# Optimization experiments

Hardware: AMD Instinct MI355X
Metric: run time of the kernel (lower is better)

The kernel has to match this reference:

```python
import jax, jax.numpy as jnp
import numpy as np

B, L, C, H, K, P = 64, 2048, 128, 128, 64, 336
NUM_BLOCKS = 4
EPS = 1e-5


def _revin_norm(x):
    mean = jnp.mean(x, axis=1, keepdims=True)
    std = jnp.sqrt(jnp.var(x, axis=1, keepdims=True) + EPS)
    return (x - mean) / std, mean, std


def _bn(x, gamma, beta, ch_axis):
    # training-mode BatchNorm1d: stats over all axes except ch_axis
    axes = tuple(i for i in range(x.ndim) if i != ch_axis)
    mean = jnp.mean(x, axis=axes, keepdims=True)
    var = jnp.var(x, axis=axes, keepdims=True)
    shp = [1] * x.ndim
    shp[ch_axis] = -1
    return (x - mean) / jnp.sqrt(var + EPS) * gamma.reshape(shp) + beta.reshape(shp)


def _mixer_block(x, bn_t_g, bn_t_b, lin_t_w, lin_t_b, bn_f_g, bn_f_b,
                 lin_f1_w, lin_f1_b, lin_f2_w, lin_f2_b):
    # timestep mixer: BN treats seq dim as channels, Linear over seq dim
    y = _bn(x, bn_t_g, bn_t_b, 1)                       # [B,L,C]
    y = jnp.swapaxes(y, 1, 2)                           # [B,C,L]
    y = jax.nn.gelu(y @ lin_t_w + lin_t_b, approximate=False)
    y = jnp.swapaxes(y, 1, 2)
    x = x + y
    # feature mixer: BN over channel dim, 2-layer MLP over features
    y = jnp.swapaxes(x, 1, 2)                           # [B,C,L]
    y = _bn(y, bn_f_g, bn_f_b, 1)
    y = jnp.swapaxes(y, 1, 2)                           # [B,L,C]
    y = jax.nn.gelu(y @ lin_f1_w + lin_f1_b, approximate=False)
    y = y @ lin_f2_w + lin_f2_b
    return x + y


def _forward(x, bern_u, cluster_embeds, wq_w, wq_b, wk_w, wk_b, wv_w, wv_b,
             cm_w1, cm_b1, cm_w2, cm_b2, tm_w1, tm_b1, tm_w2, tm_b2,
             bn_t_g, bn_t_b, lin_t_w, lin_t_b, bn_f_g, bn_f_b,
             lin_f1_w, lin_f1_b, lin_f2_w, lin_f2_b, out_w, out_b):
    xn, _, _ = _revin_norm(x)                           # [B,L,C]
    # channel MLP -> token embeddings h_i
    h = jax.nn.relu(xn @ cm_w1 + cm_b1) @ cm_w2 + cm_b2  # [B,L,H]
    # cosine-similarity soft routing to codebook
    hn = h / (jnp.linalg.norm(h, axis=-1, keepdims=True) + 1e-8)
    cn = cluster_embeds / (jnp.linalg.norm(cluster_embeds, axis=-1, keepdims=True) + 1e-8)
    p = jax.nn.softmax(jnp.einsum('blh,kh->blk', hn, cn), axis=-1)   # [B,L,K]
    M = (bern_u < p).astype(x.dtype)                    # bernoulli sample via external uniforms
    # exp-attention between cluster queries and token keys, masked by M
    Q = cluster_embeds @ wq_w + wq_b                    # [K,H]
    Km = h @ wk_w + wk_b                                # [B,L,H]
    V = h @ wv_w + wv_b                                 # [B,L,H]
    scores = jnp.einsum('kh,blh->bkl', Q, Km) / jnp.sqrt(jnp.asarray(H, x.dtype))
    aw = jax.nn.softmax(jnp.exp(scores) * jnp.swapaxes(M, 1, 2), axis=-1)  # [B,K,L]
    ao = jnp.einsum('bkl,blh->bkh', aw, V)              # [B,K,H]
    upd = ao * jnp.mean(p, axis=1)[:, :, None]          # prob-weighted cluster update
    new_cluster_embeds = jnp.mean(upd, axis=0)          # [K,H] (EMA-style copy target)
    # temporal module on channel embeddings
    h2 = jax.nn.relu(h @ tm_w1 + tm_b1) @ tm_w2 + tm_b2  # [B,L,H], H==C
    z, mean2, std2 = _revin_norm(h2)                    # second 'norm' overwrites stats
    for _ in range(NUM_BLOCKS):
        z = _mixer_block(z, bn_t_g, bn_t_b, lin_t_w, lin_t_b,
                         bn_f_g, bn_f_b, lin_f1_w, lin_f1_b, lin_f2_w, lin_f2_b)
    y = jnp.swapaxes(jnp.swapaxes(z, 1, 2) @ out_w + out_b, 1, 2)    # [B,P,C]
    y = y * std2 + mean2                                # denorm with second-call stats
    return y, new_cluster_embeds


def setup_inputs() -> dict:
    key = jax.random.key(0)
    ks = iter(jax.random.split(key, 40))

    def lin_w(fan_in, shape):
        return jax.random.uniform(next(ks), shape, jnp.float32, -1.0, 1.0) / np.sqrt(fan_in).astype(np.float32)

    return {
        'x': jax.random.normal(next(ks), (B, L, C), jnp.float32),
        'bern_u': jax.random.uniform(next(ks), (B, L, K), jnp.float32),
        'cluster_embeds': jax.random.normal(next(ks), (K, H), jnp.float32),
        'wq_w': lin_w(H, (H, H)), 'wq_b': lin_w(H, (H,)),
        'wk_w': lin_w(H, (H, H)), 'wk_b': lin_w(H, (H,)),
        'wv_w': lin_w(H, (H, H)), 'wv_b': lin_w(H, (H,)),
        'cm_w1': lin_w(C, (C, H)), 'cm_b1': lin_w(C, (H,)),
        'cm_w2': lin_w(H, (H, H)), 'cm_b2': lin_w(H, (H,)),
        'tm_w1': lin_w(H, (H, H)), 'tm_b1': lin_w(H, (H,)),
        'tm_w2': lin_w(H, (H, H)), 'tm_b2': lin_w(H, (H,)),
        'bn_t_g': jnp.ones((L,), jnp.float32), 'bn_t_b': jnp.zeros((L,), jnp.float32),
        'lin_t_w': lin_w(L, (L, L)), 'lin_t_b': lin_w(L, (L,)),
        'bn_f_g': jnp.ones((C,), jnp.float32), 'bn_f_b': jnp.zeros((C,), jnp.float32),
        'lin_f1_w': lin_w(C, (C, H)), 'lin_f1_b': lin_w(C, (H,)),
        'lin_f2_w': lin_w(H, (H, C)), 'lin_f2_b': lin_w(H, (C,)),
        'out_w': lin_w(L, (L, P)), 'out_b': lin_w(L, (P,)),
    }


def reference(x, bern_u, cluster_embeds, wq_w, wq_b, wk_w, wk_b, wv_w, wv_b,
              cm_w1, cm_b1, cm_w2, cm_b2, tm_w1, tm_b1, tm_w2, tm_b2,
              bn_t_g, bn_t_b, lin_t_w, lin_t_b, bn_f_g, bn_f_b,
              lin_f1_w, lin_f1_b, lin_f2_w, lin_f2_b, out_w, out_b):
    return _forward(x, bern_u, cluster_embeds, wq_w, wq_b, wk_w, wk_b, wv_w, wv_b,
                    cm_w1, cm_b1, cm_w2, cm_b2, tm_w1, tm_b1, tm_w2, tm_b2,
                    bn_t_g, bn_t_b, lin_t_w, lin_t_b, bn_f_g, bn_f_b,
                    lin_f1_w, lin_f1_b, lin_f2_w, lin_f2_b, out_w, out_b)
```

## Files before the change

### kernel.cpp

```cpp
#include <hip/hip_runtime.h>
#include <math.h>

#define BB 64
#define LL 2048
#define CC 128
#define HH 128
#define KK 64
#define PP 336
#define EPSf 1e-5f

typedef __attribute__((ext_vector_type(8))) short short8v;
typedef __attribute__((ext_vector_type(4))) float float4v;

__device__ inline ushort f2bf(float f) {
    union { float f; unsigned u; } v; v.f = f;
    unsigned r = (v.u + 0x7FFFu + ((v.u >> 16) & 1u)) >> 16;
    return (ushort)r;
}
__device__ inline float bf2f(ushort h) {
    union { unsigned u; float f; } v; v.u = ((unsigned)h) << 16;
    return v.f;
}

__device__ inline float fast_gelu(float v) {
// ... 119 lines not shown
            *(float4*)&Ws[kr][nc] = v;
        }
        __syncthreads();
        #pragma unroll
        for (int k = 0; k < 32; ++k) {
            float a[8], w[8];
            *(float4*)&a[0] = *(const float4*)&As[k][ty * 8];
            *(float4*)&a[4] = *(const float4*)&As[k][ty * 8 + 4];
            *(float4*)&w[0] = *(const float4*)&Ws[k][tx * 4];
            *(float4*)&w[4] = *(const float4*)&Ws[k][64 + tx * 4];
            #pragma unroll
            for (int i = 0; i < 8; ++i)
                #pragma unroll
                for (int j = 0; j < 8; ++j)
                    acc[i][j] = fmaf(a[i], w[j], acc[i][j]);
        }
    }

    #pragma unroll
    for (int i = 0; i < 8; ++i) {
        int m = m0 + ty * 8 + i;
        if (m >= M) continue;
        #pragma unroll
        for (int jj = 0; jj < 8; jj += 4) {
            int n = n0 + (jj ? 64 + tx * 4 : tx * 4);
            if (n >= N) continue;
            float o[4];
            #pragma unroll
            for (int j = 0; j < 4; ++j)
                o[j] = acc[i][jj + j] + (bias ? bias[n + j] : 0.f);
            *(float4*)(Out + (size_t)m * ldo + n) = *(float4*)o;
        }
    }
}

template <int NORM, int ACT, int EP>
__global__ __launch_bounds__(512)
void mfma_sq_kernel(const float* __restrict__ A, const ushort* __restrict__ Whi,
                    const ushort* __restrict__ Wlo, const float* __restrict__ bias,
                    float* Out,
                    const float* __restrict__ nmu, const float* __restrict__ ns,
                    const float* __restrict__ nt, int normStride,
                    ushort* __restrict__ hbOut) {
    __shared__ ushort Ahi[128][72];
    __shared__ ushort Alo[128][72];
    __shared__ ushort Bhi[128][72];
    __shared__ ushort Blo[128][72];
    int tid = threadIdx.x;
    int m0 = blockIdx.x * 128;
    int noff = (NORM == 1) ? (m0 / LL) * normStride : 0;

    int w = tid >> 6, lane = tid & 63;
    int wm = (w >> 1) * 32, wn = (w & 1) * 64;
    int col = lane & 15, kq = lane >> 4;

    float4v acc[2][4];
    #pragma unroll
    for (int i = 0; i < 2; ++i)
        #pragma unroll
        for (int j = 0; j < 4; ++j) acc[i][j] = (float4v){0.f, 0.f, 0.f, 0.f};

    for (int kt = 0; kt < 2; ++kt) {
        __syncthreads();
        #pragma unroll
        for (int it = 0; it < 2; ++it) {
            int q = tid + it * 512;
            int row = q >> 3, k0 = (q & 7) * 8;
            int kg = kt * 64 + k0;
            const float* ap = A + (size_t)(m0 + row) * 128 + kg;
            float vv[8];
            *(float4*)&vv[0] = *(const float4*)ap;
            *(float4*)&vv[4] = *(const float4*)(ap + 4);
            ushort hi[8], lo[8];
            #pragma unroll
            for (int j = 0; j < 8; ++j) {
                float v = vv[j];
                if (NORM == 1) v = (v - nmu[noff + kg + j]) * ns[noff + kg + j];
                if (NORM == 2) v = (v - nmu[kg + j]) * ns[kg + j] + nt[kg + j];
                ushort h = f2bf(v);
                hi[j] = h;
                lo[j] = f2bf(v - bf2f(h));
            }
            if (hbOut)
                *(short8v*)(hbOut + (size_t)(m0 + row) * 128 + kg) = *(short8v*)hi;
            *(short8v*)&Ahi[row][k0] = *(short8v*)hi;
            *(short8v*)&Alo[row][k0] = *(short8v*)lo;
        }
        #pragma unroll
        for (int it = 0; it < 2; ++it) {
            int q = tid + it * 512;
            int row = q >> 3, k0 = (q & 7) * 8;
            *(short8v*)&Bhi[row][k0] =
                *(const short8v*)(Whi + (size_t)row * 128 + kt * 64 + k0);
            *(short8v*)&Blo[row][k0] =
                *(const short8v*)(Wlo + (size_t)row * 128 + kt * 64 + k0);
        }
        __syncthreads();
        #pragma unroll
        for (int ksub = 0; ksub < 2; ++ksub) {
            short8v ah[2], al[2], bh[4], bl[4];
            #pragma unroll
            for (int mf = 0; mf < 2; ++mf) {
                ah[mf] = *(const short8v*)&Ahi[wm + mf * 16 + col][ksub * 32 + kq * 8];
                al[mf] = *(const short8v*)&Alo[wm + mf * 16 + col][ksub * 32 + kq * 8];
            }
            #pragma unroll
            for (int nf = 0; nf < 4; ++nf) {
                bh[nf] = *(const short8v*)&Bhi[wn + nf * 16 + col][ksub * 32 + kq * 8];
                bl[nf] = *(const short8v*)&Blo[wn + nf * 16 + col][ksub * 32 + kq * 8];
            }
            #pragma unroll
            for (int mf = 0; mf < 2; ++mf)
                #pragma unroll
                for (int nf = 0; nf < 4; ++nf)
                    acc[mf][nf] = __builtin_amdgcn_mfma_f32_16x16x32_bf16(
                        ah[mf], bh[nf], acc[mf][nf], 0, 0, 0);
            #pragma unroll
            for (int mf = 0; mf < 2; ++mf)
                #pragma unroll
                for (int nf = 0; nf < 4; ++nf)
                    acc[mf][nf] = __builtin_amdgcn_mfma_f32_16x16x32_bf16(
                        ah[mf], bl[nf], acc[mf][nf], 0, 0, 0);
            #pragma unroll
            for (int mf = 0; mf < 2; ++mf)
                #pragma unroll
                for (int nf = 0; nf < 4; ++nf)
                    acc[mf][nf] = __builtin_amdgcn_mfma_f32_16x16x32_bf16(
                        al[mf], bh[nf], acc[mf][nf], 0, 0, 0);
        }
    }

    int rbase = kq * 4;
    #pragma unroll
    for (int nf = 0; nf < 4; ++nf) {
        int n = wn + nf * 16 + col;
        if (EP == 2 && n >= 64) continue;
        float bn = bias ? bias[n] : 0.f;
        #pragma unroll
        for (int mf = 0; mf < 2; ++mf) {
            #pragma unroll
            for (int r = 0; r < 4; ++r) {
                int m = m0 + wm + mf * 16 + rbase + r;
                float v = acc[mf][nf][r] + bn;
                if (ACT == 1) v = fmaxf(v, 0.f);
                if (ACT == 2) v = fast_gelu(v);
                if (EP == 0) Out[(size_t)m * 128 + n] = v;
                else if (EP == 1) Out[(size_t)m * 128 + n] += v;
                else Out[(size_t)m * 64 + n] = v;
            }
        }
    }
}

template <int NORM, int ACT1, int ACT2, int EP2, int PREC>
__global__ __launch_bounds__(512)
void mfma_sq2_kernel(const float* __restrict__ A,
                     const ushort* __restrict__ W1h, const ushort* __restrict__ W1l,
                     const float* __restrict__ b1v,
                     const ushort* __restrict__ W2h, const ushort* __restrict__ W2l,
                     const float* __restrict__ b2v, float* Out,
                     const float* __restrict__ nmu, const float* __restrict__ ns,
                     const float* __restrict__ nt, int normStride,
                     float* __restrict__ rsum, float* __restrict__ rsq) {
    __shared__ ushort Xhi[128][72];
    __shared__ ushort Xlo[PREC ? 128 : 1][72];
    __shared__ ushort Bh[128][72];
    __shared__ ushort Bl[PREC ? 128 : 1][72];
    int tid = threadIdx.x;
    int m0 = blockIdx.x * 128;
    int noff = (NORM == 1) ? (m0 / LL) * normStride : 0;
    int w = tid >> 6, lane = tid & 63;
    int wm = (w >> 1) * 32, wn = (w & 1) * 64;
    int col = lane & 15, kq = lane >> 4;

    float4v acc[2][4];
    #pragma unroll
    for (int i = 0; i < 2; ++i)
        #pragma unroll
        for (int j = 0; j < 4; ++j) acc[i][j] = (float4v){0.f, 0.f, 0.f, 0.f};

    for (int kt = 0; kt < 2; ++kt) {
        __syncthreads();
        #pragma unroll
        for (int it = 0; it < 2; ++it) {
            int q = tid + it * 512;
            int row = q >> 3, k0 = (q & 7) * 8;
            int kg = kt * 64 + k0;
            const float* ap = A + (size_t)(m0 + row) * 128 + kg;
            float vv[8];
            *(float4*)&vv[0] = *(const float4*)ap;
            *(float4*)&vv[4] = *(const float4*)(ap + 4);
            ushort hi[8], lo[8];
            #pragma unroll
            for (int j = 0; j < 8; ++j) {
                float v = vv[j];
                if (NORM == 1) v = (v - nmu[noff + kg + j]) * ns[noff + kg + j];
                if (NORM == 2) v = (v - nmu[kg + j]) * ns[kg + j] + nt[kg + j];
                ushort h = f2bf(v);
                hi[j] = h;
                if (PREC) lo[j] = f2bf(v - bf2f(h));
            }
            *(short8v*)&Xhi[row][k0] = *(short8v*)hi;
            if (PREC) *(short8v*)&Xlo[row][k0] = *(short8v*)lo;
        }
        #pragma unroll
        for (int it = 0; it < 2; ++it) {
            int q = tid + it * 512;
            int row = q >> 3, k0 = (q & 7) * 8;
            *(short8v*)&Bh[row][k0] =
                *(const short8v*)(W1h + (size_t)row * 128 + kt * 64 + k0);
            if (PREC)
                *(short8v*)&Bl[row][k0] =
                    *(const short8v*)(W1l + (size_t)row * 128 + kt * 64 + k0);
        }
        __syncthreads();
        #pragma unroll
        for (int ksub = 0; ksub < 2; ++ksub) {
            short8v ah[2], al[2], bh[4], bl[4];
            #pragma unroll
            for (int mf = 0; mf < 2; ++mf) {
                ah[mf] = *(const short8v*)&Xhi[wm + mf * 16 + col][ksub * 32 + kq * 8];
                if (PREC) al[mf] = *(const short8v*)&Xlo[wm + mf * 16 + col][ksub * 32 + kq * 8];
            }
            #pragma unroll
            for (int nf = 0; nf < 4; ++nf) {
                bh[nf] = *(const short8v*)&Bh[wn + nf * 16 + col][ksub * 32 + kq * 8];
                if (PREC) bl[nf] = *(const short8v*)&Bl[wn + nf * 16 + col][ksub * 32 + kq * 8];
            }
            #pragma unroll
            for (int mf = 0; mf < 2; ++mf)
                #pragma unroll
                for (int nf = 0; nf < 4; ++nf)
                    acc[mf][nf] = __builtin_amdgcn_mfma_f32_16x16x32_bf16(
                        ah[mf], bh[nf], acc[mf][nf], 0, 0, 0);
            if (PREC) {
                #pragma unroll
                for (int mf = 0; mf < 2; ++mf)
                    #pragma unroll
                    for (int nf = 0; nf < 4; ++nf)
                        acc[mf][nf] = __builtin_amdgcn_mfma_f32_16x16x32_bf16(
                            ah[mf], bl[nf], acc[mf][nf], 0, 0, 0);
                #pragma unroll
                for (int mf = 0; mf < 2; ++mf)
                    #pragma unroll
                    for (int nf = 0; nf < 4; ++nf)
                        acc[mf][nf] = __builtin_amdgcn_mfma_f32_16x16x32_bf16(
                            al[mf], bh[nf], acc[mf][nf], 0, 0, 0);
            }
        }
    }

    float4v acc2[2][4];
    #pragma unroll
    for (int i = 0; i < 2; ++i)
        #pragma unroll
        for (int j = 0; j < 4; ++j) acc2[i][j] = (float4v){0.f, 0.f, 0.f, 0.f};

    for (int kt2 = 0; kt2 < 2; ++kt2) {
        __syncthreads();
        if ((wn >> 6) == kt2) {
            #pragma unroll
            for (int nf = 0; nf < 4; ++nf) {
                float bn = b1v[wn + nf * 16 + col];
                #pragma unroll
                for (int mf = 0; mf < 2; ++mf) {
                    #pragma unroll
                    for (int r = 0; r < 4; ++r) {
                        float v = acc[mf][nf][r] + bn;
                        if (ACT1 == 1) v = fmaxf(v, 0.f);
                        if (ACT1 == 2) v = fast_gelu(v);
                        int row = wm + mf * 16 + kq * 4 + r;
                        int c2 = nf * 16 + col;
                        ushort h = f2bf(v);
                        Xhi[row][c2] = h;
                        if (PREC) Xlo[row][c2] = f2bf(v - bf2f(h));
                    }
                }
            }
        }
        #pragma unroll
        for (int it = 0; it < 2; ++it) {
            int q = tid + it * 512;
            int row = q >> 3, k0 = (q & 7) * 8;
            *(short8v*)&Bh[row][k0] =
                *(const short8v*)(W2h + (size_t)row * 128 + kt2 * 64 + k0);
            if (PREC)
                *(short8v*)&Bl[row][k0] =
                    *(const short8v*)(W2l + (size_t)row * 128 + kt2 * 64 + k0);
        }
        __syncthreads();
        #pragma unroll
        for (int ksub = 0; ksub < 2; ++ksub) {
            short8v ah[2], al[2], bh[4], bl[4];
            #pragma unroll
            for (int mf = 0; mf < 2; ++mf) {
                ah[mf] = *(const short8v*)&Xhi[wm + mf * 16 + col][ksub * 32 + kq * 8];
                if (PREC) al[mf] = *(const short8v*)&Xlo[wm + mf * 16 + col][ksub * 32 + kq * 8];
            }
            #pragma unroll
            for (int nf = 0; nf < 4; ++nf) {
                bh[nf] = *(const short8v*)&Bh[wn + nf * 16 + col][ksub * 32 + kq * 8];
                if (PREC) bl[nf] = *(const short8v*)&Bl[wn + nf * 16 + col][ksub * 32 + kq * 8];
            }
            #pragma unroll
            for (int mf = 0; mf < 2; ++mf)
                #pragma unroll
                for (int nf = 0; nf < 4; ++nf)
                    acc2[mf][nf] = __builtin_amdgcn_mfma_f32_16x16x32_bf16(
                        ah[mf], bh[nf], acc2[mf][nf], 0, 0, 0);
            if (PREC) {
                #pragma unroll
                for (int mf = 0; mf < 2; ++mf)
                    #pragma unroll
                    for (int nf = 0; nf < 4; ++nf)
                        acc2[mf][nf] = __builtin_amdgcn_mfma_f32_16x16x32_bf16(
                            ah[mf], bl[nf], acc2[mf][nf], 0, 0, 0);
                #pragma unroll
                for (int mf = 0; mf < 2; ++mf)
                    #pragma unroll
                    for (int nf = 0; nf < 4; ++nf)
                        acc2[mf][nf] = __builtin_amdgcn_mfma_f32_16x16x32_bf16(
                            al[mf], bh[nf], acc2[mf][nf], 0, 0, 0);
            }
        }
    }

    int rbase = kq * 4;
    float rs_[2][4];
    float rq_[2][4];
    float cs_[4], cq_[4];
    if (EP2 == 1 || EP2 == 3) {
        #pragma unroll
        for (int a = 0; a < 2; ++a)
            #pragma unroll
            for (int b = 0; b < 4; ++b) { rs_[a][b] = 0.f; rq_[a][b] = 0.f; }
    }
    if (EP2 == 2) {
        #pragma unroll
        for (int a = 0; a < 4; ++a) { cs_[a] = 0.f; cq_[a] = 0.f; }
    }
    #pragma unroll
    for (int nf = 0; nf < 4; ++nf) {
        int n = wn + nf * 16 + col;
        float bn = b2v[n];
        #pragma unroll
        for (int mf = 0; mf < 2; ++mf) {
            #pragma unroll
            for (int r = 0; r < 4; ++r) {
                int m = m0 + wm + mf * 16 + rbase + r;
                float v = acc2[mf][nf][r] + bn;
                if (ACT2 == 1) v = fmaxf(v, 0.f);
                if (ACT2 == 2) v = fast_gelu(v);
                if (EP2 == 1) {
                    float fin = Out[(size_t)m * 128 + n] + v;
                    Out[(size_t)m * 128 + n] = fin;
                    rs_[mf][r] += fin;
                    rq_[mf][r] += fin * fin;
                } else {
                    Out[(size_t)m * 128 + n] = v;
                    if (EP2 == 2) { cs_[nf] += v; cq_[nf] += v * v; }
                    if (EP2 == 3) rq_[mf][r] += v * v;
                }
            }
        }
    }
    if (EP2 == 1) {
        #pragma unroll
        for (int mf = 0; mf < 2; ++mf)
            #pragma unroll
            for (int r = 0; r < 4; ++r) {
                float s = rs_[mf][r], q = rq_[mf][r];
                #pragma unroll
                for (int o = 1; o <= 8; o <<= 1) {
                    s += __shfl_xor(s, o);
                    q += __shfl_xor(q, o);
                }
                rs_[mf][r] = s; rq_[mf][r] = q;
            }
        __syncthreads();
        float* sred = (float*)&Xhi[0][0];
        float* qred = sred + 256;
        if (col == 0) {
            #pragma unroll
            for (int mf = 0; mf < 2; ++mf)
                #pragma unroll
                for (int r = 0; r < 4; ++r) {
                    int row = wm + mf * 16 + kq * 4 + r;
                    sred[row * 2 + (wn >> 6)] = rs_[mf][r];
                    qred[row * 2 + (wn >> 6)] = rq_[mf][r];
                }
        }
        __syncthreads();
        if (tid < 128) {
            rsum[(size_t)m0 + tid] = sred[tid * 2] + sred[tid * 2 + 1];
            rsq[(size_t)m0 + tid]  = qred[tid * 2] + qred[tid * 2 + 1];
        }
    }
    if (EP2 == 3) {
        #pragma unroll
        for (int mf = 0; mf < 2; ++mf)
            #pragma unroll
            for (int r = 0; r < 4; ++r) {
                float q = rq_[mf][r];
                #pragma unroll
                for (int o = 1; o <= 8; o <<= 1) q += __shfl_xor(q, o);
                rq_[mf][r] = q;
            }
        __syncthreads();
        float* qred = (float*)&Xhi[0][0];
        if (col == 0) {
            #pragma unroll
            for (int mf = 0; mf < 2; ++mf)
                #pragma unroll
                for (int r = 0; r < 4; ++r) {
                    int row = wm + mf * 16 + kq * 4 + r;
                    qred[row * 2 + (wn >> 6)] = rq_[mf][r];
                }
        }
        __syncthreads();
        if (tid < 128)
            rsq[(size_t)m0 + tid] = qred[tid * 2] + qred[tid * 2 + 1];
    }
    if (EP2 == 2) {
        #pragma unroll
        for (int nf = 0; nf < 4; ++nf) {
            #pragma unroll
            for (int o = 16; o <= 32; o <<= 1) {
                cs_[nf] += __shfl_xor(cs_[nf], o);
                cq_[nf] += __shfl_xor(cq_[nf], o);
            }
        }
        __syncthreads();
        float* colS = (float*)&Xhi[0][0];
        float* colQ = colS + 512;
        if (kq == 0) {
            #pragma unroll
            for (int nf = 0; nf < 4; ++nf) {
                int n = wn + nf * 16 + col;
                colS[(wm >> 5) * 128 + n] = cs_[nf];
                colQ[(wm >> 5) * 128 + n] = cq_[nf];
            }
        }
        __syncthreads();
        if (tid < 128) {
            rsum[(size_t)blockIdx.x * 256 + tid] =
                (colS[tid] + colS[128 + tid]) + (colS[256 + tid] + colS[384 + tid]);
            rsum[(size_t)blockIdx.x * 256 + 128 + tid] =
                (colQ[tid] + colQ[128 + tid]) + (colQ[256 + tid] + colQ[384 + tid]);
        }
    }
}

__global__ void wsplit_kernel(const float* __restrict__ W, ushort* __restrict__ Whi,
                              ushort* __restrict__ Wlo) {
    __shared__ float t[32][33];
    int k0 = blockIdx.x * 32, n0 = blockIdx.y * 32;
    int tx = threadIdx.x, ty = threadIdx.y;
    for (int i = ty; i < 32; i += 8)
        t[i][tx] = W[(size_t)(k0 + i) * 128 + n0 + tx];
    __syncthreads();
    for (int i = ty; i < 32; i += 8) {
        float v = t[tx][i];
        ushort h = f2bf(v);
        Whi[(size_t)(n0 + i) * 128 + k0 + tx] = h;
        Wlo[(size_t)(n0 + i) * 128 + k0 + tx] = f2bf(v - bf2f(h));
    }
}

__global__ __launch_bounds__(512)
void mfma_ts5_kernel(const ushort* __restrict__ A, const ushort* __restrict__ W,
                     const float* __restrict__ bias, float* Z,
                     int nx, int nwg, float* __restrict__ bnfP) {
    __shared__ __align__(16) ushort smem[32768];
    float (*Ol)[132] = (float(*)[132])smem;

    int bid = blockIdx.x;
    int cpx = nwg >> 3;
    int swz = (bid & 7) * cpx + (bid >> 3);
    int n0 = (swz % nx) * 128;
    int m0 = (swz / nx) * 128;

    int tid = threadIdx.x;
    int w = tid >> 6, lane = tid & 63;
    int wm = (w >> 1) * 32, wn = (w & 1) * 64;
    int col = lane & 15, kq = lane >> 4;

    int srow = lane >> 3;
    int scol = ((lane & 7) ^ srow) << 3;
    int xr = (col & 7) << 4;

    float4v acc[2][4];
    #pragma unroll
    for (int i = 0; i < 2; ++i)
        #pragma unroll
        for (int j = 0; j < 4; ++j) acc[i][j] = (float4v){0.f, 0.f, 0.f, 0.f};

    const int Kd = LL;
    const int kTiles = 32;

    #pragma unroll
    for (int it = 0; it < 2; ++it) {
        int rb = (w << 4) + (it << 3);
        async16(A + (size_t)(m0 + rb + srow) * Kd + scol, smem + (rb << 6));
        async16(W + (size_t)(n0 + rb + srow) * Kd + scol, smem + 8192 + (rb << 6));
    }
    __syncthreads();

    for (int kt = 0; kt < kTiles; ++kt) {
        int cur = kt & 1;
        const ushort* Ac = smem + (cur << 14);
        const ushort* Bc = Ac + 8192;
        if (kt + 1 < kTiles) {
            ushort* An = smem + ((cur ^ 1) << 14);
            ushort* Bn = An + 8192;
            int kb = (kt + 1) << 6;
            #pragma unroll
            for (int it = 0; it < 2; ++it) {
                int rb = (w << 4) + (it << 3);
                async16(A + (size_t)(m0 + rb + srow) * Kd + kb + scol, An + (rb << 6));
                async16(W + (size_t)(n0 + rb + srow) * Kd + kb + scol, Bn + (rb << 6));
            }
        }
        __builtin_amdgcn_s_setprio(1);
        #pragma unroll
        for (int ksub = 0; ksub < 2; ++ksub) {
            int cswz = (((ksub << 6) + (kq << 4)) ^ xr) >> 1;
            short8v af[2], bf[4];
            #pragma unroll
            for (int mf = 0; mf < 2; ++mf)
                af[mf] = *(const short8v*)(Ac + (wm + mf * 16 + col) * 64 + cswz);
            #pragma unroll
            for (int nf = 0; nf < 4; ++nf)
                bf[nf] = *(const short8v*)(Bc + (wn + nf * 16 + col) * 64 + cswz);
            #pragma unroll
            for (int mf = 0; mf < 2; ++mf)
                #pragma unroll
                for (int nf = 0; nf < 4; ++nf)
                    acc[mf][nf] = __builtin_amdgcn_mfma_f32_16x16x32_bf16(
                        af[mf], bf[nf], acc[mf][nf], 0, 0, 0);
        }
        __builtin_amdgcn_s_setprio(0);
        __syncthreads();
    }

    int b = m0 >> 7;
    float cs[8], cq[8];
    #pragma unroll
    for (int j = 0; j < 8; ++j) { cs[j] = 0.f; cq[j] = 0.f; }
// ... 33 lines not shown
        }
    }
    __syncthreads();
    float* sred = (float*)smem;
    float* qred = sred + 4096;
    #pragma unroll
    for (int j = 0; j < 8; ++j) {
        sred[nloc * 128 + c0 + j] = cs[j];
        qred[nloc * 128 + c0 + j] = cq[j];
    }
    __syncthreads();
    if (tid < 128) {
        float a = 0.f;
        for (int r = 0; r < 32; ++r) a += sred[r * 128 + tid];
        bnfP[(size_t)bid * 256 + tid] = a;
    } else if (tid < 256) {
        int c = tid - 128;
        float a = 0.f;
        for (int r = 0; r < 32; ++r) a += qred[r * 128 + c];
        bnfP[(size_t)bid * 256 + 128 + c] = a;
    }
}

template <int EPM>
__global__ __launch_bounds__(512)
void mfma_g8_kernel(const ushort* __restrict__ A, const ushort* __restrict__ W,
                    const float* __restrict__ bias, float* Z,
                    int N, int Kd, int LDO, int nx, int nwg,
                    const float* __restrict__ epS, const float* __restrict__ epM) {
    __shared__ __align__(16) ushort smem[32768];
    float (*Ol)[132] = (float(*)[132])smem;

    int bid = blockIdx.x;
    int cpx = nwg >> 3;
    int swz = (bid & 7) * cpx + (bid >> 3);
    int n0 = (swz % nx) * 128;
    int m0 = (swz / nx) * 128;

    int tid = threadIdx.x;
    int w = tid >> 6, lane = tid & 63;
    int wm = (w >> 1) * 32, wn = (w & 1) * 64;
    int col = lane & 15, kq = lane >> 4;

    int srow = lane >> 3;
    int scol = ((lane & 7) ^ srow) << 3;
    int xr = (col & 7) << 4;

    float4v acc[2][4];
    #pragma unroll
    for (int i = 0; i < 2; ++i)
        #pragma unroll
        for (int j = 0; j < 4; ++j) acc[i][j] = (float4v){0.f, 0.f, 0.f, 0.f};

    int kTiles = Kd >> 6;

    #pragma unroll
    for (int it = 0; it < 2; ++it) {
        int rb = (w << 4) + (it << 3);
        async16(A + (size_t)(m0 + rb + srow) * Kd + scol, smem + (rb << 6));
        async16(W + (size_t)(n0 + rb + srow) * Kd + scol, smem + 8192 + (rb << 6));
    }
    __syncthreads();

    for (int kt = 0; kt < kTiles; ++kt) {
        int cur = kt & 1;
        const ushort* Ac = smem + (cur << 14);
        const ushort* Bc = Ac + 8192;
        if (kt + 1 < kTiles) {
            ushort* An = smem + ((cur ^ 1) << 14);
            ushort* Bn = An + 8192;
            int kb = (kt + 1) << 6;
            #pragma unroll
            for (int it = 0; it < 2; ++it) {
                int rb = (w << 4) + (it << 3);
                async16(A + (size_t)(m0 + rb + srow) * Kd + kb + scol, An + (rb << 6));
                async16(W + (size_t)(n0 + rb + srow) * Kd + kb + scol, Bn + (rb << 6));
            }
        }
        __builtin_amdgcn_s_setprio(1);
        #pragma unroll
        for (int ksub = 0; ksub < 2; ++ksub) {
            int cswz = (((ksub << 6) + (kq << 4)) ^ xr) >> 1;
            short8v af[2], bf[4];
            #pragma unroll
            for (int mf = 0; mf < 2; ++mf)
                af[mf] = *(const short8v*)(Ac + (wm + mf * 16 + col) * 64 + cswz);
            #pragma unroll
            for (int nf = 0; nf < 4; ++nf)
                bf[nf] = *(const short8v*)(Bc + (wn + nf * 16 + col) * 64 + cswz);
            #pragma unroll
            for (int mf = 0; mf < 2; ++mf)
                #pragma unroll
                for (int nf = 0; nf < 4; ++nf)
                    acc[mf][nf] = __builtin_amdgcn_mfma_f32_16x16x32_bf16(
                        af[mf], bf[nf], acc[mf][nf], 0, 0, 0);
        }
        __builtin_amdgcn_s_setprio(0);
        __syncthreads();
    }

    int b = m0 >> 7;
    int nloc = tid >> 4, c0 = (tid & 15) * 8;
    #pragma unroll
    for (int q = 0; q < 4; ++q) {
        __syncthreads();
        #pragma unroll
        for (int nf = 0; nf < 4; ++nf) {
            int gnl = wn + nf * 16;
            if ((gnl >> 5) != q) continue;
            int gn = n0 + gnl + col;
            float bn = (EPM == 2 && gn >= N) ? 0.f : bias[gn];
            int nl = gnl - q * 32 + col;
            #pragma unroll
            for (int mf = 0; mf < 2; ++mf)
                #pragma unroll
                for (int r = 0; r < 4; ++r)
                    Ol[nl][wm + mf * 16 + kq * 4 + r] = acc[mf][nf][r] + bn;
        }
        __syncthreads();
        int gn = n0 + q * 32 + nloc;
        if (gn >= N) continue;
        float* zr;
        if (EPM == 3)
            zr = Z + (((size_t)(m0 >> 11) * 64 + gn) * 2048) + (m0 & 2047) + c0;
        else
            zr = Z + ((size_t)b * LDO + gn) * CC + c0;
        #pragma unroll
        for (int i = 0; i < 2; ++i) {
            float4 v = *(float4*)&Ol[nloc][c0 + i * 4];
            if (EPM == 2) {
                int mb = m0 + c0 + i * 4;
                float4 s4 = *(const float4*)(epS + mb);
                float4 m4 = *(const float4*)(epM + mb);
                v.x = v.x * s4.x + m4.x; v.y = v.y * s4.y + m4.y;
                v.z = v.z * s4.z + m4.z; v.w = v.w * s4.w + m4.w;
            }
            *(float4*)(zr + i * 4) = v;
        }
    }
}

__global__ void wtrans_kernel(const float* __restrict__ W, ushort* __restrict__ WT,
                              int Kd, int N) {
    __shared__ float t[32][33];
    int k0 = blockIdx.x * 32, n0 = blockIdx.y * 32;
    int tx = threadIdx.x, ty = threadIdx.y;
    for (int i = ty; i < 32; i += 8) {
        int n = n0 + tx;
        t[i][tx] = (n < N) ? W[(size_t)(k0 + i) * N + n] : 0.f;
    }
    __syncthreads();
    for (int i = ty; i < 32; i += 8)
        WT[(size_t)(n0 + i) * Kd + k0 + tx] = f2bf(t[tx][i]);
}

__global__ void cn_split_kernel(const float* __restrict__ ce, ushort* __restrict__ ch,
                                ushort* __restrict__ cl) {
    int k = blockIdx.x, h = threadIdx.x;
    if (k >= KK) {
        ch[(size_t)k * 128 + h] = 0;
        cl[(size_t)k * 128 + h] = 0;
        return;
    }
    __shared__ float sh[128];
    float v = ce[(size_t)k * HH + h];
    sh[h] = v * v;
    __syncthreads();
    for (int o = 64; o >= 1; o >>= 1) {
        if (h < o) sh[h] += sh[h + o];
        __syncthreads();
    }
    float nv = v / (sqrtf(sh[0]) + 1e-8f);
    ushort hh = f2bf(nv);
    ch[(size_t)k * 128 + h] = hh;
    cl[(size_t)k * 128 + h] = f2bf(nv - bf2f(hh));
}

__global__ void qprime_kernel(const float* __restrict__ Q, const float* __restrict__ wk_w,
                              const float* __restrict__ wk_b, ushort* __restrict__ qpb,
                              float* __restrict__ qbp) {
    int k = blockIdx.x;
    int hp = threadIdx.x;
    if (k >= KK) {
        qpb[(size_t)k * HH + hp] = 0;
        if (hp == 0) qbp[k] = 0.f;
        return;
    }
    __shared__ float qrow[128];
    __shared__ float red[128];
    qrow[hp] = Q[(size_t)k * HH + hp];
    __syncthreads();
    float s = 0.f;
    for (int h = 0; h < HH; ++h) s = fmaf(qrow[h], wk_w[(size_t)hp * HH + h], s);
    const float rs = 0.088388347648318447f;
    qpb[(size_t)k * HH + hp] = f2bf(s * rs);
    red[hp] = qrow[hp] * wk_b[hp];
    __syncthreads();
    for (int o = 64; o >= 1; o >>= 1) {
        if (hp < o) red[hp] += red[hp + o];
        __syncthreads();
    }
    if (hp == 0) qbp[k] = red[0] * rs;
}

__global__ __launch_bounds__(256)
void pmask_kernel(const float* __restrict__ sp, const float* __restrict__ rn,
                  const float* __restrict__ bern, unsigned char* __restrict__ Mt,
                  float* __restrict__ ppart) {
    int b = blockIdx.y;
    int l0 = blockIdx.x * 32;
    int tid = threadIdx.x;
    int wv = tid >> 6, lane = tid & 63;
    __shared__ float Msh[64][33];
    __shared__ float psum[4][64];
    float pa = 0.f;
    for (int tt = 0; tt < 8; ++tt) {
        int l = l0 + wv * 8 + tt;
        size_t tok = (size_t)b * LL + l;
        float s = sp[tok * 64 + lane] * rn[tok];
        float mx = s;
        #pragma unroll
        for (int o = 32; o >= 1; o >>= 1) mx = fmaxf(mx, __shfl_xor(mx, o));
        float ev = expf(s - mx);
        float sm = ev;
        #pragma unroll
        for (int o = 32; o >= 1; o >>= 1) sm += __shfl_xor(sm, o);
        float p = ev / sm;
        pa += p;
        Msh[lane][wv * 8 + tt] = (bern[tok * KK + lane] < p) ? 1.f : 0.f;
    }
    psum[wv][lane] = pa;
    __syncthreads();
    for (int q = tid; q < 64 * 32; q += 256) {
        int k = q >> 5, j = q & 31;
        Mt[((size_t)b * KK + k) * LL + l0 + j] = (unsigned char)Msh[k][j];
    }
    if (tid < 64)
        ppart[((size_t)b * (LL / 32) + blockIdx.x) * KK + tid] =
            psum[0][tid] + psum[1][tid] + psum[2][tid] + psum[3][tid];
}

__global__ void pmean_final_kernel(const float* __restrict__ part, float* __restrict__ pm) {
    int b = blockIdx.x, k = threadIdx.x;
    float s = 0.f;
    for (int i = 0; i < LL / 32; ++i) s += part[((size_t)b * (LL / 32) + i) * KK + k];
    pm[b * KK + k] = s * (1.f / LL);
}

__global__ __launch_bounds__(256)
void aw_kernel(float* __restrict__ S, const unsigned char* __restrict__ Mt) {
    size_t base = (size_t)blockIdx.x * LL;
    int tid = threadIdx.x;
    float t[8];
    float mx = -1e30f;
    #pragma unroll
    for (int i = 0; i < 8; ++i) {
        int l = tid + i * 256;
        float v = expf(S[base + l]) * (float)Mt[base + l];
        t[i] = v;
        mx = fmaxf(mx, v);
    }
    __shared__ float shA[4];
    __shared__ float shB[4];
    #pragma unroll
    for (int o = 32; o >= 1; o >>= 1) mx = fmaxf(mx, __shfl_xor(mx, o));
    if ((tid & 63) == 0) shA[tid >> 6] = mx;
    __syncthreads();
    mx = fmaxf(fmaxf(shA[0], shA[1]), fmaxf(shA[2], shA[3]));
    float e[8];
    float sum = 0.f;
    #pragma unroll
    for (int i = 0; i < 8; ++i) { e[i] = expf(t[i] - mx); sum += e[i]; }
    #pragma unroll
    for (int o = 32; o >= 1; o >>= 1) sum += __shfl_xor(sum, o);
    if ((tid & 63) == 0) shB[tid >> 6] = sum;
    __syncthreads();
    sum = (shB[0] + shB[1]) + (shB[2] + shB[3]);
    float inv = 1.f / sum;
    #pragma unroll
    for (int i = 0; i < 8; ++i) S[base + tid + i * 256] = e[i] * inv;
}

__global__ __launch_bounds__(256)
void awh_part_kernel(const float* __restrict__ AWs, const float* __restrict__ hmat,
                     float* __restrict__ part) {
    __shared__ float AT[32][64];
    __shared__ float VT[32][128];
    int b = blockIdx.y, sp = blockIdx.x;
    int tid = threadIdx.x;
    int tx = tid & 15, ty = tid >> 4;
    float acc[4][8] = {};
    const float* Ab = AWs + (size_t)b * KK * LL + sp * 512;
    const float* Vb = hmat + ((size_t)b * LL + sp * 512) * HH;
    for (int lt = 0; lt < 512; lt += 32) {
        __syncthreads();
        #pragma unroll
        for (int it = 0; it < 2; ++it) {
            int q = tid + it * 256;
            int row = q >> 3;
            int lq = (q & 7) << 2;
            float4 v = *(const float4*)(Ab + (size_t)row * LL + lt + lq);
            AT[lq][row] = v.x; AT[lq + 1][row] = v.y;
            AT[lq + 2][row] = v.z; AT[lq + 3][row] = v.w;
        }
        #pragma unroll
        for (int it = 0; it < 4; ++it) {
            int q = tid + it * 256;
            int lr = q >> 5;
            int hc = (q & 31) << 2;
            *(float4*)&VT[lr][hc] = *(const float4*)(Vb + (size_t)(lt + lr) * HH + hc);
        }
        __syncthreads();
        #pragma unroll
        for (int l = 0; l < 32; ++l) {
            float av[4], vv[8];
            *(float4*)&av[0] = *(const float4*)&AT[l][ty * 4];
            *(float4*)&vv[0] = *(const float4*)&VT[l][tx * 4];
            *(float4*)&vv[4] = *(const float4*)&VT[l][64 + tx * 4];
            #pragma unroll
            for (int i = 0; i < 4; ++i)
                #pragma unroll
                for (int j = 0; j < 8; ++j)
                    acc[i][j] = fmaf(av[i], vv[j], acc[i][j]);
        }
    }
    #pragma unroll
    for (int i = 0; i < 4; ++i) {
        int k = ty * 4 + i;
        #pragma unroll
        for (int jj = 0; jj < 8; jj += 4) {
            int h = (jj ? 64 + tx * 4 : tx * 4);
            float o[4];
            #pragma unroll
            for (int j = 0; j < 4; ++j) o[j] = acc[i][jj + j];
            *(float4*)(part + (((size_t)b * 4 + sp) * KK + k) * HH + h) = *(float4*)o;
        }
    }
}

__global__ void awh_reduce_kernel(const float* __restrict__ part, float* __restrict__ awh) {
    int bk = blockIdx.x, h = threadIdx.x;
    int b = bk >> 6, k = bk & 63;
    float s = 0.f;
    #pragma unroll
    for (int sp = 0; sp < 4; ++sp)
        s += part[(((size_t)b * 4 + sp) * KK + k) * HH + h];
    awh[(size_t)bk * HH + h] = s;
}

__global__ void newce_kernel(const float* __restrict__ ao, const float* __restrict__ pm,
                             float* __restrict__ outTail) {
    int k = blockIdx.x, h = threadIdx.x;
    float s = 0.f;
    for (int b = 0; b < BB; ++b)
        s += ao[((size_t)b * KK + k) * HH + h] * pm[b * KK + k];
    outTail[(size_t)k * HH + h] = s * (1.f / BB);
}

__global__ void revin_apply_kernel(const float* __restrict__ in, float* __restrict__ out,
                                   const float* __restrict__ mu, const float* __restrict__ rs,
                                   float* __restrict__ rsum, float* __restrict__ rsq) {
    int b = blockIdx.y;
    size_t base = (size_t)b * LL * CC + (size_t)blockIdx.x * 8192;
    int c0 = (threadIdx.x * 4) & 127;
    int lane = threadIdx.x & 63;
    float4 m4 = *(const float4*)(mu + b * CC + c0);
    float4 r4 = *(const float4*)(rs + b * CC + c0);
    #pragma unroll
    for (int j = 0; j < 8; ++j) {
        float4 v = *(const float4*)(in + base + threadIdx.x * 4 + j * 1024);
        v.x = (v.x - m4.x) * r4.x; v.y = (v.y - m4.y) * r4.y;
        v.z = (v.z - m4.z) * r4.z; v.w = (v.w - m4.w) * r4.w;
        *(float4*)(out + base + threadIdx.x * 4 + j * 1024) = v;
        float s = v.x + v.y + v.z + v.w;
        float q = v.x * v.x + v.y * v.y + v.z * v.z + v.w * v.w;
        #pragma unroll
        for (int o = 1; o <= 16; o <<= 1) {
            s += __shfl_xor(s, o);
            q += __shfl_xor(q, o);
        }
        if ((lane & 31) == 0) {
            size_t row = (base + (size_t)threadIdx.x * 4 + (size_t)j * 1024) >> 7;
            rsum[row] = s;
            rsq[row] = q;
        }
    }
}

__global__ void bnt_final_kernel(const float* __restrict__ rsum, const float* __restrict__ rsq,
                                 float* __restrict__ mu, float* __restrict__ rv) {
    int l = blockIdx.x * 256 + threadIdx.x;
    float s = 0.f, q = 0.f;
    for (int b = 0; b < BB; ++b) {
        s += rsum[(size_t)b * LL + l];
        q += rsq[(size_t)b * LL + l];
    }
    float m = s * (1.f / (BB * CC));
    float var = q * (1.f / (BB * CC)) - m * m;
    var = fmaxf(var, 0.f);
    mu[l] = m;
    rv[l] = 1.f / sqrtf(var + EPSf);
}

template <bool DO_BN>
__global__ __launch_bounds__(256)
void transpose_bn_kernel(const float* __restrict__ in, ushort* __restrict__ out,
                         const float* __restrict__ mu, const float* __restrict__ rv,
                         const float* __restrict__ g, const float* __restrict__ be) {
    __shared__ ushort tile[32][72];
    int l0 = blockIdx.x * 64, c0 = blockIdx.y * 32, b = blockIdx.z;
    int t = threadIdx.x;
    const float* ib = in + ((size_t)b * LL + l0) * CC + c0;
    #pragma unroll
    for (int it = 0; it < 2; ++it) {
        int idx = t + it * 256;
        int row = idx >> 3;
        int c = (idx & 7) * 4;
        float4 v = *(const float4*)(ib + (size_t)row * CC + c);
        if (DO_BN) {
            int l = l0 + row;
            float sc = rv[l] * g[l];
            float m = mu[l], bb = be[l];
            v.x = (v.x - m) * sc + bb; v.y = (v.y - m) * sc + bb;
            v.z = (v.z - m) * sc + bb; v.w = (v.w - m) * sc + bb;
        }
        tile[c    ][row] = f2bf(v.x);
        tile[c + 1][row] = f2bf(v.y);
        tile[c + 2][row] = f2bf(v.z);
        tile[c + 3][row] = f2bf(v.w);
    }
    __syncthreads();
    int cc = t >> 3, l8 = (t & 7) * 8;
    ushort* ob = out + (size_t)b * CC * LL + (size_t)(c0 + cc) * LL + l0 + l8;
    *(uint4*)ob = *(const uint4*)&tile[cc][l8];
}

__global__ void bnf_mid_kernel(const float* __restrict__ part, float* __restrict__ mid) {
    int gblk = blockIdx.x, t = threadIdx.x;
    float s = 0.f;
    #pragma unroll
    for (int i = 0; i < 16; ++i)
        s += part[(size_t)(gblk * 16 + i) * 256 + t];
    mid[(size_t)gblk * 256 + t] = s;
}

__global__ void bnf_final_kernel(const float* __restrict__ mid, const float* __restrict__ g,
                                 const float* __restrict__ be, float* __restrict__ mu,
                                 float* __restrict__ sA, float* __restrict__ tA) {
    int c = threadIdx.x;
    float s = 0.f, s2 = 0.f;
    #pragma unroll
    for (int i = 0; i < 64; ++i) {
        s += mid[(size_t)i * 256 + c];
        s2 += mid[(size_t)i * 256 + 128 + c];
    }
    float m = s / (float)(BB * LL);
    float var = s2 / (float)(BB * LL) - m * m;
    var = fmaxf(var, 0.f);
    float rvv = 1.f / sqrtf(var + EPSf);
    mu[c] = m;
    sA[c] = rvv * g[c];
    tA[c] = be[c];
}

extern "C" void kernel_launch(void* const* d_in, const int* in_sizes, int n_in,
                              void* d_out, int out_size, void* d_ws, size_t ws_size,
                              hipStream_t stream) {
    const float* x     = (const float*)d_in[0];
    const float* bern  = (const float*)d_in[1];
    const float* ce    = (const float*)d_in[2];
    const float* wq_w  = (const float*)d_in[3];
    const float* wq_b  = (const float*)d_in[4];
    const float* wk_w  = (const float*)d_in[5];
    const float* wk_b  = (const float*)d_in[6];
    const float* wv_w  = (const float*)d_in[7];
    const float* wv_b  = (const float*)d_in[8];
    const float* cm_w1 = (const float*)d_in[9];
    const float* cm_b1 = (const float*)d_in[10];
    const float* cm_w2 = (const float*)d_in[11];
    const float* cm_b2 = (const float*)d_in[12];
    const float* tm_w1 = (const float*)d_in[13];
    const float* tm_b1 = (const float*)d_in[14];
    const float* tm_w2 = (const float*)d_in[15];
    const float* tm_b2 = (const float*)d_in[16];
    const float* bn_t_g = (const float*)d_in[17];
    const float* bn_t_b = (const float*)d_in[18];
    const float* lin_t_w = (const float*)d_in[19];
    const float* lin_t_b = (const float*)d_in[20];
    const float* bn_f_g = (const float*)d_in[21];
    const float* bn_f_b = (const float*)d_in[22];
    const float* f1_w  = (const float*)d_in[23];
    const float* f1_b  = (const float*)d_in[24];
    const float* f2_w  = (const float*)d_in[25];
    const float* f2_b  = (const float*)d_in[26];
    const float* out_w = (const float*)d_in[27];
    const float* out_b = (const float*)d_in[28];
    (void)in_sizes; (void)n_in; (void)out_size;

    float* y = (float*)d_out;
    float* ceOut = y + (size_t)BB * PP * CC;

    float* ws = (float*)d_ws;
    size_t off = 0;
    auto alloc = [&](size_t n) { float* p = ws + off; off += n; return p; };
    float* mean1  = alloc(BB * CC);
    float* rstd1  = alloc(BB * CC);
    float* std1   = alloc(BB * CC);
    float* mean2  = alloc(BB * CC);
    float* rstd2  = alloc(BB * CC);
    float* std2   = alloc(BB * CC);
    float* bnmu   = alloc(LL);
    float* bnrv   = alloc(LL);
    float* bfpart = alloc(1024 * 256);
    float* bfmid  = alloc(64 * 256);
    float* bfmu   = alloc(CC);
    float* bfs    = alloc(CC);
    float* bft    = alloc(CC);
    float* cxpart = alloc(BB * 8 * 256);
    float* cpart2 = alloc(1024 * 256);
    float* qbuf   = alloc(KK * HH);
    ushort* qpb   = (ushort*)alloc(128 * 128 / 2);
    float* qbp    = alloc(128);
    ushort* cnbh  = (ushort*)alloc(8192);
    ushort* cnbl  = (ushort*)alloc(8192);
    float* rn     = alloc((size_t)BB * LL);
    float* rsum   = alloc((size_t)BB * LL);
    float* rsq    = alloc((size_t)BB * LL);
    float* ppart  = alloc((size_t)BB * (LL / 32) * KK);
    float* pmean  = alloc(BB * KK);
    float* awhprt = alloc((size_t)BB * 4 * KK * HH);
    float* awh    = alloc((size_t)BB * KK * HH);
    float* aobuf  = alloc((size_t)BB * KK * HH);
    ushort* wsp   = (ushort*)alloc(7 * 2 * 16384 / 2);
    ushort* wtT   = (ushort*)alloc((size_t)LL * LL / 2);
    ushort* owT   = (ushort*)alloc((size_t)384 * LL / 2);
    float* S      = alloc((size_t)BB * KK * LL);
    float* buf0   = alloc((size_t)BB * LL * CC);
    float* buf2   = alloc((size_t)BB * LL * CC);
    unsigned char* Mt = (unsigned char*)(ws + off);
    ushort* abf = (ushort*)S;
    ushort* hb  = (ushort*)buf0;
    (void)ws_size;

    auto whi = [&](int i) { return wsp + (size_t)i * 2 * 16384; };
    auto wlo = [&](int i) { return wsp + (size_t)i * 2 * 16384 + 16384; };

    const int ML = BB * LL;
    dim3 tb(32, 8);
    dim3 tgrid(LL / 64, CC / 32, BB);
    dim3 wsg(4, 4);

    wtrans_kernel<<<dim3(LL / 32, LL / 32), tb, 0, stream>>>(lin_t_w, wtT, LL, LL);
    wtrans_kernel<<<dim3(LL / 32, 12), tb, 0, stream>>>(out_w, owT, LL, PP);
    wsplit_kernel<<<wsg, tb, 0, stream>>>(cm_w1, whi(0), wlo(0));
    wsplit_kernel<<<wsg, tb, 0, stream>>>(cm_w2, whi(1), wlo(1));
    wsplit_kernel<<<wsg, tb, 0, stream>>>(tm_w1, whi(2), wlo(2));
    wsplit_kernel<<<wsg, tb, 0, stream>>>(tm_w2, whi(3), wlo(3));
    wsplit_kernel<<<wsg, tb, 0, stream>>>(f1_w, whi(4), wlo(4));
    wsplit_kernel<<<wsg, tb, 0, stream>>>(f2_w, whi(5), wlo(5));
    wsplit_kernel<<<wsg, tb, 0, stream>>>(wv_w, whi(6), wlo(6));

    colstats_part_kernel<<<dim3(8, BB), 256, 0, stream>>>(x, cxpart);
    colstats_final_kernel<<<dim3(BB), dim3(128), 0, stream>>>(cxpart, mean1, rstd1, std1);
    mfma_sq2_kernel<1, 1, 0, 3, 1><<<dim3(ML / 128), 512, 0, stream>>>(
        x, whi(0), wlo(0), cm_b1, whi(1), wlo(1), cm_b2, buf2, mean1, rstd1, nullptr, CC,
        nullptr, rsq);
    rn_final_kernel<<<dim3(ML / 256), 256, 0, stream>>>(rsq, rn);
    gemm_kernel<<<dim3(1, 1), 256, 0, stream>>>(ce, wq_w, wq_b, qbuf,
        KK, HH, HH, HH, HH, HH);
    qprime_kernel<<<dim3(128), dim3(128), 0, stream>>>(qbuf, wk_w, wk_b, qpb, qbp);
    cn_split_kernel<<<dim3(128), dim3(128), 0, stream>>>(ce, cnbh, cnbl);
    mfma_sq_kernel<0, 0, 2><<<dim3(ML / 128), 512, 0, stream>>>(
        buf2, cnbh, cnbl, nullptr, S, nullptr, nullptr, nullptr, 0, hb);
    pmask_kernel<<<dim3(LL / 32, BB), 256, 0, stream>>>(S, rn, bern, Mt, ppart);
    pmean_final_kernel<<<dim3(BB), dim3(64), 0, stream>>>(ppart, pmean);
    mfma_g8_kernel<3><<<dim3(1024), 512, 0, stream>>>(
        hb, qpb, qbp, S, KK, 128, 0, 1, 1024, nullptr, nullptr);
    aw_kernel<<<dim3(BB * KK), 256, 0, stream>>>(S, Mt);
    awh_part_kernel<<<dim3(4, BB), 256, 0, stream>>>(S, buf2, awhprt);
    awh_reduce_kernel<<<dim3(BB * KK), dim3(128), 0, stream>>>(awhprt, awh);
    mfma_sq_kernel<0, 0, 0><<<dim3((BB * KK) / 128), 512, 0, stream>>>(
        awh, whi(6), wlo(6), wv_b, aobuf, nullptr, nullptr, nullptr, 0, nullptr);
    newce_kernel<<<dim3(KK), dim3(128), 0, stream>>>(aobuf, pmean, ceOut);
    mfma_sq2_kernel<0, 1, 0, 2, 1><<<dim3(ML / 128), 512, 0, stream>>>(
        buf2, whi(2), wlo(2), tm_b1, whi(3), wlo(3), tm_b2, buf0,
        nullptr, nullptr, nullptr, 0, cpart2, nullptr);
    colstats2_final_kernel<<<dim3(BB), dim3(128), 0, stream>>>(cpart2, mean2, rstd2, std2);
    revin_apply_kernel<<<dim3(32, BB), 256, 0, stream>>>(buf0, buf2, mean2, rstd2, rsum, rsq);
    for (int blkI = 0; blkI < 4; ++blkI) {
        bnt_final_kernel<<<dim3(8), 256, 0, stream>>>(rsum, rsq, bnmu, bnrv);
        transpose_bn_kernel<true><<<tgrid, 256, 0, stream>>>(buf2, abf, bnmu, bnrv, bn_t_g, bn_t_b);
        mfma_ts5_kernel<<<dim3(1024), 512, 0, stream>>>(
            abf, wtT, lin_t_b, buf2, 16, 1024, bfpart);
        bnf_mid_kernel<<<dim3(64), 256, 0, stream>>>(bfpart, bfmid);
        bnf_final_kernel<<<dim3(1), dim3(128), 0, stream>>>(bfmid, bn_f_g, bn_f_b, bfmu, bfs, bft);
        mfma_sq2_kernel<2, 2, 0, 1, 0><<<dim3(ML / 128), 512, 0, stream>>>(
            buf2, whi(4), wlo(4), f1_b, whi(5), wlo(5), f2_b, buf2, bfmu, bfs, bft, 0,
            rsum, rsq);
    }
    transpose_bn_kernel<false><<<tgrid, 256, 0, stream>>>(buf2, abf,
        nullptr, nullptr, nullptr, nullptr);
    mfma_g8_kernel<2><<<dim3(192), 512, 0, stream>>>(
        abf, owT, out_b, y, PP, LL, PP, 3, 192, std2, mean2);
}
```

Measured before the change: 1.161 ms.

## Fold timestep BatchNorm into weights and emit transposed bf16 from feature-mixer epilogue

The per-block timestep BatchNorm scale is folded into a per-iteration scaled copy of the transposed lin_t weight, and its shift into a precomputed bias (W·shift + b). The raw activation therefore no longer needs normalizing. The feature-mixer MLP epilogue now writes the transposed bf16 activation directly through a shared-memory tile. This removes the separate transpose_bn pass over the full B·L·C tensor in each block. In exchange, each block rescales the 2048x2048 bf16 weight (reading and writing about 8MB) and does an extra bias reduction, and the scale is rounded into bf16 weights, which slightly changes numerics.

```diff
diff --git a/kernel.cpp b/kernel.cpp
--- a/kernel.cpp
+++ b/kernel.cpp
@@ -295,7 +295,7 @@
     }
 }
 
-template <int NORM, int ACT1, int ACT2, int EP2, int PREC>
+template <int NORM, int ACT1, int ACT2, int EP2, int PREC, int EMITT>
 __global__ __launch_bounds__(512)
 void mfma_sq2_kernel(const float* __restrict__ A,
                      const ushort* __restrict__ W1h, const ushort* __restrict__ W1l,
@@ -304,11 +304,13 @@
                      const float* __restrict__ b2v, float* Out,
                      const float* __restrict__ nmu, const float* __restrict__ ns,
                      const float* __restrict__ nt, int normStride,
-                     float* __restrict__ rsum, float* __restrict__ rsq) {
+                     float* __restrict__ rsum, float* __restrict__ rsq,
+                     ushort* __restrict__ abfT) {
     __shared__ ushort Xhi[128][72];
     __shared__ ushort Xlo[PREC ? 128 : 1][72];
     __shared__ ushort Bh[128][72];
     __shared__ ushort Bl[PREC ? 128 : 1][72];
+    __shared__ ushort Tbuf[EMITT ? 128 : 1][136];
     int tid = threadIdx.x;
     int m0 = blockIdx.x * 128;
     int noff = (NORM == 1) ? (m0 / LL) * normStride : 0;
@@ -497,6 +499,7 @@
                 if (EP2 == 1) {
                     float fin = Out[(size_t)m * 128 + n] + v;
                     Out[(size_t)m * 128 + n] = fin;
+                    if (EMITT) Tbuf[n][wm + mf * 16 + rbase + r] = f2bf(fin);
                     rs_[mf][r] += fin;
                     rq_[mf][r] += fin * fin;
                 } else {
@@ -537,6 +540,16 @@
         if (tid < 128) {
             rsum[(size_t)m0 + tid] = sred[tid * 2] + sred[tid * 2 + 1];
             rsq[(size_t)m0 + tid]  = qred[tid * 2] + qred[tid * 2 + 1];
+        }
+        if (EMITT) {
+            int bT = m0 >> 11, l0 = m0 & 2047;
+            #pragma unroll
+            for (int it = 0; it < 4; ++it) {
+                int idx = tid + it * 512;
+                int cr = idx >> 4, u = (idx & 15) * 8;
+                *(uint4*)(abfT + ((size_t)bT * CC + cr) * LL + l0 + u) =
+                    *(const uint4*)&Tbuf[cr][u];
+            }
         }
     }
     if (EP2 == 3) {
@@ -876,6 +889,41 @@
     __syncthreads();
     for (int i = ty; i < 32; i += 8)
         WT[(size_t)(n0 + i) * Kd + k0 + tx] = f2bf(t[tx][i]);
+}
+
+__global__ void wtfold_kernel(const ushort* __restrict__ wtT, const float* __restrict__ sc,
+                              ushort* __restrict__ wtTs) {
+    int n = blockIdx.x;
+    int l = threadIdx.x * 8;
+    ushort u[8];
+    *(uint4*)u = *(const uint4*)(wtT + (size_t)n * LL + l);
+    float4 s0 = *(const float4*)(sc + l);
+    float4 s1 = *(const float4*)(sc + l + 4);
+    u[0] = f2bf(bf2f(u[0]) * s0.x); u[1] = f2bf(bf2f(u[1]) * s0.y);
+    u[2] = f2bf(bf2f(u[2]) * s0.z); u[3] = f2bf(bf2f(u[3]) * s0.w);
+    u[4] = f2bf(bf2f(u[4]) * s1.x); u[5] = f2bf(bf2f(u[5]) * s1.y);
+    u[6] = f2bf(bf2f(u[6]) * s1.z); u[7] = f2bf(bf2f(u[7]) * s1.w);
+    *(uint4*)(wtTs + (size_t)n * LL + l) = *(uint4*)u;
+}
+
+__global__ void tbias_kernel(const ushort* __restrict__ wtT, const float* __restrict__ shift,
+                             const float* __restrict__ tb, float* __restrict__ bn2) {
+    int n = blockIdx.x;
+    int t = threadIdx.x;
+    int l = t * 8;
+    ushort u[8];
+    *(uint4*)u = *(const uint4*)(wtT + (size_t)n * LL + l);
+    float4 s0 = *(const float4*)(shift + l);
+    float4 s1 = *(const float4*)(shift + l + 4);
+    float p = bf2f(u[0]) * s0.x + bf2f(u[1]) * s0.y + bf2f(u[2]) * s0.z +
+              bf2f(u[3]) * s0.w + bf2f(u[4]) * s1.x + bf2f(u[5]) * s1.y +
+              bf2f(u[6]) * s1.z + bf2f(u[7]) * s1.w;
+    #pragma unroll
+    for (int o = 1; o <= 32; o <<= 1) p += __shfl_xor(p, o);
+    __shared__ float red[4];
+    if ((t & 63) == 0) red[t >> 6] = p;
+    __syncthreads();
+    if (t == 0) bn2[n] = tb[n] + red[0] + red[1] + red[2] + red[3];
 }
 
 __global__ void cn_split_kernel(const float* __restrict__ ce, ushort* __restrict__ ch,
@@ -1112,7 +1160,8 @@
 }
 
 __global__ void bnt_final_kernel(const float* __restrict__ rsum, const float* __restrict__ rsq,
-                                 float* __restrict__ mu, float* __restrict__ rv) {
+                                 const float* __restrict__ g, const float* __restrict__ be,
+                                 float* __restrict__ scv, float* __restrict__ shv) {
     int l = blockIdx.x * 256 + threadIdx.x;
     float s = 0.f, q = 0.f;
     for (int b = 0; b < BB; ++b) {
@@ -1122,8 +1171,10 @@
     float m = s * (1.f / (BB * CC));
     float var = q * (1.f / (BB * CC)) - m * m;
     var = fmaxf(var, 0.f);
-    mu[l] = m;
-    rv[l] = 1.f / sqrtf(var + EPSf);
+    float rv = 1.f / sqrtf(var + EPSf);
+    float sc = rv * g[l];
+    scv[l] = sc;
+    shv[l] = be[l] - m * sc;
 }
 
 template <bool DO_BN>
@@ -1233,8 +1284,9 @@
     float* mean2  = alloc(BB * CC);
     float* rstd2  = alloc(BB * CC);
     float* std2   = alloc(BB * CC);
-    float* bnmu   = alloc(LL);
-    float* bnrv   = alloc(LL);
+    float* bnsc   = alloc(LL);
+    float* bnsh   = alloc(LL);
+    float* bn2    = alloc(LL);
     float* bfpart = alloc(1024 * 256);
     float* bfmid  = alloc(64 * 256);
     float* bfmu   = alloc(CC);
@@ -1257,6 +1309,7 @@
     float* aobuf  = alloc((size_t)BB * KK * HH);
     ushort* wsp   = (ushort*)alloc(7 * 2 * 16384 / 2);
     ushort* wtT   = (ushort*)alloc((size_t)LL * LL / 2);
+    ushort* wtTs  = (ushort*)alloc((size_t)LL * LL / 2);
     ushort* owT   = (ushort*)alloc((size_t)384 * LL / 2);
     float* S      = alloc((size_t)BB * KK * LL);
     float* buf0   = alloc((size_t)BB * LL * CC);
@@ -1286,9 +1339,9 @@
 
     colstats_part_kernel<<<dim3(8, BB), 256, 0, stream>>>(x, cxpart);
     colstats_final_kernel<<<dim3(BB), dim3(128), 0, stream>>>(cxpart, mean1, rstd1, std1);
-    mfma_sq2_kernel<1, 1, 0, 3, 1><<<dim3(ML / 128), 512, 0, stream>>>(
+    mfma_sq2_kernel<1, 1, 0, 3, 1, 0><<<dim3(ML / 128), 512, 0, stream>>>(
         x, whi(0), wlo(0), cm_b1, whi(1), wlo(1), cm_b2, buf2, mean1, rstd1, nullptr, CC,
-        nullptr, rsq);
+        nullptr, rsq, nullptr);
     rn_final_kernel<<<dim3(ML / 256), 256, 0, stream>>>(rsq, rn);
     gemm_kernel<<<dim3(1, 1), 256, 0, stream>>>(ce, wq_w, wq_b, qbuf,
         KK, HH, HH, HH, HH, HH);
@@ -1306,24 +1359,25 @@
     mfma_sq_kernel<0, 0, 0><<<dim3((BB * KK) / 128), 512, 0, stream>>>(
         awh, whi(6), wlo(6), wv_b, aobuf, nullptr, nullptr, nullptr, 0, nullptr);
     newce_kernel<<<dim3(KK), dim3(128), 0, stream>>>(aobuf, pmean, ceOut);
-    mfma_sq2_kernel<0, 1, 0, 2, 1><<<dim3(ML / 128), 512, 0, stream>>>(
+    mfma_sq2_kernel<0, 1, 0, 2, 1, 0><<<dim3(ML / 128), 512, 0, stream>>>(
         buf2, whi(2), wlo(2), tm_b1, whi(3), wlo(3), tm_b2, buf0,
-        nullptr, nullptr, nullptr, 0, cpart2, nullptr);
+        nullptr, nullptr, nullptr, 0, cpart2, nullptr, nullptr);
     colstats2_final_kernel<<<dim3(BB), dim3(128), 0, stream>>>(cpart2, mean2, rstd2, std2);
     revin_apply_kernel<<<dim3(32, BB), 256, 0, stream>>>(buf0, buf2, mean2, rstd2, rsum, rsq);
+    transpose_bn_kernel<false><<<tgrid, 256, 0, stream>>>(buf2, abf,
+        nullptr, nullptr, nullptr, nullptr);
     for (int blkI = 0; blkI < 4; ++blkI) {
-        bnt_final_kernel<<<dim3(8), 256, 0, stream>>>(rsum, rsq, bnmu, bnrv);
-        transpose_bn_kernel<true><<<tgrid, 256, 0, stream>>>(buf2, abf, bnmu, bnrv, bn_t_g, bn_t_b);
+        bnt_final_kernel<<<dim3(8), 256, 0, stream>>>(rsum, rsq, bn_t_g, bn_t_b, bnsc, bnsh);
+        wtfold_kernel<<<dim3(LL), 256, 0, stream>>>(wtT, bnsc, wtTs);
+        tbias_kernel<<<dim3(LL), 256, 0, stream>>>(wtT, bnsh, lin_t_b, bn2);
         mfma_ts5_kernel<<<dim3(1024), 512, 0, stream>>>(
-            abf, wtT, lin_t_b, buf2, 16, 1024, bfpart);
+            abf, wtTs, bn2, buf2, 16, 1024, bfpart);
         bnf_mid_kernel<<<dim3(64), 256, 0, stream>>>(bfpart, bfmid);
         bnf_final_kernel<<<dim3(1), dim3(128), 0, stream>>>(bfmid, bn_f_g, bn_f_b, bfmu, bfs, bft);
-        mfma_sq2_kernel<2, 2, 0, 1, 0><<<dim3(ML / 128), 512, 0, stream>>>(
+        mfma_sq2_kernel<2, 2, 0, 1, 0, 1><<<dim3(ML / 128), 512, 0, stream>>>(
             buf2, whi(4), wlo(4), f1_b, whi(5), wlo(5), f2_b, buf2, bfmu, bfs, bft, 0,
-            rsum, rsq);
-    }
-    transpose_bn_kernel<false><<<tgrid, 256, 0, stream>>>(buf2, abf,
-        nullptr, nullptr, nullptr, nullptr);
+            rsum, rsq, abf);
+    }
     mfma_g8_kernel<2><<<dim3(192), 512, 0, stream>>>(
         abf, owT, out_b, y, PP, LL, PP, 3, 192, std2, mean2);
 }
```

Result: faster. 1.110 ms (-4.4%).
